# Kernel optimization log

Hardware: AMD Instinct MI355X
Metric: run time of the kernel (lower is better)

## Reference

```python
import jax, jax.numpy as jnp
import numpy as np

EPS = 1e-5

def _layernorm(h, g, b):
    mu = jnp.mean(h, axis=-1, keepdims=True)
    var = jnp.mean(jnp.square(h - mu), axis=-1, keepdims=True)
    return (h - mu) * jax.lax.rsqrt(var + EPS) * g + b

def setup_inputs() -> dict:
    key = jax.random.key(0)
    ks = jax.random.split(key, 16)
    N, E, H = 100000, 500000, 128
    x = jax.random.normal(ks[0], (N, H), dtype=jnp.float32)
    edge_index = jax.random.randint(ks[1], (2, E), 0, N, dtype=jnp.int64)
    edge = jax.random.normal(ks[2], (E, H), dtype=jnp.float32)
    def lin(k, fan_in, fan_out):
        bound = 1.0 / np.sqrt(fan_in)
        k1, k2 = jax.random.split(k)
        W = jax.random.uniform(k1, (fan_in, fan_out), jnp.float32, -bound, bound)
        b = jax.random.uniform(k2, (fan_out,), jnp.float32, -bound, bound)
        return W, b
    W0, b0 = lin(ks[3], 3 * H, H)
    W1, b1 = lin(ks[4], H, H)
    W2, b2 = lin(ks[5], H, H)
    W3, b3 = lin(ks[6], H, 1)
    g0 = jnp.ones((H,), jnp.float32); be0 = jnp.zeros((H,), jnp.float32)
    g1 = jnp.ones((H,), jnp.float32); be1 = jnp.zeros((H,), jnp.float32)
    g2 = jnp.ones((H,), jnp.float32); be2 = jnp.zeros((H,), jnp.float32)
    return dict(x=x, edge_index=edge_index, edge=edge,
                W0=W0, b0=b0, g0=g0, be0=be0,
                W1=W1, b1=b1, g1=g1, be1=be1,
                W2=W2, b2=b2, g2=g2, be2=be2,
                W3=W3, b3=b3)

def reference(x, edge_index, edge, W0, b0, g0, be0, W1, b1, g1, be1, W2, b2, g2, be2, W3, b3):
    src, dst = edge_index[0], edge_index[1]
    # gather + concat: [E, 3*H]
    h = jnp.concatenate([x[src], x[dst], edge], axis=-1)
    h = jax.nn.relu(_layernorm(h @ W0 + b0, g0, be0))
    h = jax.nn.relu(_layernorm(h @ W1 + b1, g1, be1))
    h = jax.nn.relu(_layernorm(h @ W2 + b2, g2, be2))
    out = h @ W3 + b3  # [E, 1]
    return jnp.squeeze(out, axis=-1)
```

## Files before the change

### kernel.cpp

```cpp
#include <hip/hip_runtime.h>

typedef _Float16 f16;
typedef _Float16 f16x8 __attribute__((ext_vector_type(8)));
typedef _Float16 f16x4 __attribute__((ext_vector_type(4)));
typedef float    f32x4 __attribute__((ext_vector_type(4)));

static constexpr int H  = 128;
static constexpr int MT = 128;
static constexpr int PC = 40;
static constexpr int PA = 136;

__global__ __launch_bounds__(256, 2)
void edge_mlp_fused(const float* __restrict__ x,
                    const int* __restrict__ eidx,
                    const float* __restrict__ edge,
                    const float* __restrict__ W0, const float* __restrict__ b0,
                    const float* __restrict__ g0, const float* __restrict__ be0,
                    const float* __restrict__ W1, const float* __restrict__ b1,
                    const float* __restrict__ g1, const float* __restrict__ be1,
                    const float* __restrict__ W2, const float* __restrict__ b2,
                    const float* __restrict__ g2, const float* __restrict__ be2,
                    const float* __restrict__ W3, const float* __restrict__ b3,
                    float* __restrict__ out, int E)
{
    __shared__ f16   achunk[MT * PC];
    __shared__ f16   wchunk[H * PC];
    __shared__ f16   act[MT * PA];
    __shared__ int   srcoff[MT];
    __shared__ int   dstoff[MT];
    __shared__ float outbuf[MT];

    const int tid  = threadIdx.x;
    const int lane = tid & 63;
    const int wid  = tid >> 6;
    const int c    = lane & 15;
    const int g    = lane >> 4;
    const int wrow = wid * 32;
    const long long e0 = (long long)blockIdx.x * MT;

    if (tid < MT) {
        long long e = e0 + tid; if (e >= E) e = (long long)E - 1;
        srcoff[tid] = eidx[e]     * (H * 4);
        dstoff[tid] = eidx[E + e] * (H * 4);
    }

    f32x4 acc[8][2];
    #pragma unroll
    for (int t = 0; t < 8; ++t) {
        acc[t][0] = f32x4{0.f, 0.f, 0.f, 0.f};
        acc[t][1] = f32x4{0.f, 0.f, 0.f, 0.f};
    }

    auto stageW = [&](const float* __restrict__ W, int k0) {
        #pragma unroll
        for (int i = 0; i < 4; ++i) {
            int f  = i * 256 + tid;
            int n  = f & 127;
            int kq = f >> 7;
            const float* p = W + (size_t)(k0 + kq * 4) * H + n;
            f16x4 v;
            v[0] = (f16)p[0];
            v[1] = (f16)p[H];
            v[2] = (f16)p[2 * H];
            v[3] = (f16)p[3 * H];
            *(f16x4*)&wchunk[n * PC + kq * 4] = v;
        }
    };

    auto mfma_tiles = [&](const f16* __restrict__ A, int astride, int koff) {
        f16x8 a0 = *(const f16x8*)&A[(wrow + c)      * astride + koff + g * 8];
        f16x8 a1 = *(const f16x8*)&A[(wrow + 16 + c) * astride + koff + g * 8];
        #pragma unroll
        for (int t = 0; t < 8; ++t) {
            f16x8 bf = *(const f16x8*)&wchunk[(t * 16 + c) * PC + g * 8];
            acc[t][0] = __builtin_amdgcn_mfma_f32_16x16x32_f16(a0, bf, acc[t][0], 0, 0, 0);
            acc[t][1] = __builtin_amdgcn_mfma_f32_16x16x32_f16(a1, bf, acc[t][1], 0, 0, 0);
        }
    };

    auto ln_relu_store = [&](const float* __restrict__ bias,
                             const float* __restrict__ gamma,
                             const float* __restrict__ beta) {
        float mu[2][4], rs[2][4];
        #pragma unroll
        for (int t = 0; t < 8; ++t) {
            float bt = bias[t * 16 + c];
            #pragma unroll
            for (int s = 0; s < 2; ++s)
                #pragma unroll
                for (int r = 0; r < 4; ++r) acc[t][s][r] += bt;
        }
        #pragma unroll
        for (int s = 0; s < 2; ++s)
            #pragma unroll
            for (int r = 0; r < 4; ++r) {
                float v = 0.f, q = 0.f;
                #pragma unroll
                for (int t = 0; t < 8; ++t) { float a = acc[t][s][r]; v += a; q += a * a; }
                #pragma unroll
                for (int m = 1; m < 16; m <<= 1) {
                    v += __shfl_xor(v, m, 64);
                    q += __shfl_xor(q, m, 64);
                }
                float mean = v * (1.0f / H);
                float var  = q * (1.0f / H) - mean * mean;
                mu[s][r] = mean;
                rs[s][r] = rsqrtf(var + 1e-5f);
            }
        __syncthreads();
        #pragma unroll
        for (int t = 0; t < 8; ++t) {
            float gm = gamma[t * 16 + c];
            float bb = beta[t * 16 + c];
            #pragma unroll
            for (int s = 0; s < 2; ++s)
                #pragma unroll
                for (int r = 0; r < 4; ++r) {
                    float v = (acc[t][s][r] - mu[s][r]) * rs[s][r] * gm + bb;
                    v = fmaxf(v, 0.f);
                    act[(wrow + s * 16 + g * 4 + r) * PA + t * 16 + c] = (f16)v;
                }
        }
        #pragma unroll
        for (int t = 0; t < 8; ++t) {
            acc[t][0] = f32x4{0.f, 0.f, 0.f, 0.f};
            acc[t][1] = f32x4{0.f, 0.f, 0.f, 0.f};
        }
    };

    for (int kc = 0; kc < 12; ++kc) {
        __syncthreads();
        {
            int r  = tid >> 1;
            int hf = tid & 1;
            int kk = (kc & 3) * 32 + hf * 16;
            const float* p;
            if (kc < 4)      p = (const float*)((const char*)x + srcoff[r]) + kk;
            else if (kc < 8) p = (const float*)((const char*)x + dstoff[r]) + kk;
            else {
                long long e = e0 + r; if (e >= E) e = (long long)E - 1;
                p = edge + e * H + kk;
            }
            float4 v0 = ((const float4*)p)[0];
            float4 v1 = ((const float4*)p)[1];
            float4 v2 = ((const float4*)p)[2];
            float4 v3 = ((const float4*)p)[3];
            f16x8 lo, hi;
            lo[0] = (f16)v0.x; lo[1] = (f16)v0.y; lo[2] = (f16)v0.z; lo[3] = (f16)v0.w;
            lo[4] = (f16)v1.x; lo[5] = (f16)v1.y; lo[6] = (f16)v1.z; lo[7] = (f16)v1.w;
            hi[0] = (f16)v2.x; hi[1] = (f16)v2.y; hi[2] = (f16)v2.z; hi[3] = (f16)v2.w;
            hi[4] = (f16)v3.x; hi[5] = (f16)v3.y; hi[6] = (f16)v3.z; hi[7] = (f16)v3.w;
            *(f16x8*)&achunk[r * PC + hf * 16]     = lo;
            *(f16x8*)&achunk[r * PC + hf * 16 + 8] = hi;
        }
        stageW(W0, kc * 32);
        __syncthreads();
        mfma_tiles(achunk, PC, 0);
    }
    ln_relu_store(b0, g0, be0);

    for (int kc = 0; kc < 4; ++kc) {
        __syncthreads();
        stageW(W1, kc * 32);
        __syncthreads();
        mfma_tiles(act, PA, kc * 32);
    }
    ln_relu_store(b1, g1, be1);

    for (int kc = 0; kc < 4; ++kc) {
        __syncthreads();
        stageW(W2, kc * 32);
        __syncthreads();
        mfma_tiles(act, PA, kc * 32);
    }

    {
        float mu[2][4], rs[2][4];
        #pragma unroll
        for (int t = 0; t < 8; ++t) {
            float bt = b2[t * 16 + c];
            #pragma unroll
            for (int s = 0; s < 2; ++s)
                #pragma unroll
                for (int r = 0; r < 4; ++r) acc[t][s][r] += bt;
        }
        #pragma unroll
        for (int s = 0; s < 2; ++s)
            #pragma unroll
            for (int r = 0; r < 4; ++r) {
                float v = 0.f, q = 0.f;
                #pragma unroll
                for (int t = 0; t < 8; ++t) { float a = acc[t][s][r]; v += a; q += a * a; }
                #pragma unroll
                for (int m = 1; m < 16; m <<= 1) {
                    v += __shfl_xor(v, m, 64);
                    q += __shfl_xor(q, m, 64);
                }
                float mean = v * (1.0f / H);
                float var  = q * (1.0f / H) - mean * mean;
                mu[s][r] = mean;
                rs[s][r] = rsqrtf(var + 1e-5f);
            }
        float po[2][4] = {{0.f,0.f,0.f,0.f},{0.f,0.f,0.f,0.f}};
        #pragma unroll
        for (int t = 0; t < 8; ++t) {
            float gm  = g2[t * 16 + c];
            float bb  = be2[t * 16 + c];
            float w3v = W3[t * 16 + c];
            #pragma unroll
            for (int s = 0; s < 2; ++s)
                #pragma unroll
                for (int r = 0; r < 4; ++r) {
                    float v = (acc[t][s][r] - mu[s][r]) * rs[s][r] * gm + bb;
                    v = fmaxf(v, 0.f);
                    po[s][r] += v * w3v;
                }
        }
        #pragma unroll
        for (int s = 0; s < 2; ++s)
            #pragma unroll
            for (int r = 0; r < 4; ++r) {
                #pragma unroll
                for (int m = 1; m < 16; m <<= 1) po[s][r] += __shfl_xor(po[s][r], m, 64);
            }
        if (c == 0) {
            #pragma unroll
            for (int s = 0; s < 2; ++s)
                #pragma unroll
                for (int r = 0; r < 4; ++r)
                    outbuf[wrow + s * 16 + g * 4 + r] = po[s][r];
        }
    }
    __syncthreads();
    if (tid < MT) {
        long long e = e0 + tid;
        if (e < E) out[e] = outbuf[tid] + b3[0];
    }
}

extern "C" void kernel_launch(void* const* d_in, const int* in_sizes, int n_in,
                              void* d_out, int out_size, void* d_ws, size_t ws_size,
                              hipStream_t stream)
{
    const float* x    = (const float*)d_in[0];
    const int*   eidx = (const int*)d_in[1];
    const float* edge = (const float*)d_in[2];
    const float* W0   = (const float*)d_in[3];
    const float* b0   = (const float*)d_in[4];
    const float* g0   = (const float*)d_in[5];
    const float* be0  = (const float*)d_in[6];
    const float* W1   = (const float*)d_in[7];
    const float* b1   = (const float*)d_in[8];
    const float* g1   = (const float*)d_in[9];
    const float* be1  = (const float*)d_in[10];
    const float* W2   = (const float*)d_in[11];
    const float* b2   = (const float*)d_in[12];
    const float* g2   = (const float*)d_in[13];
    const float* be2  = (const float*)d_in[14];
    const float* W3   = (const float*)d_in[15];
    const float* b3   = (const float*)d_in[16];
    float*       out  = (float*)d_out;

    const int E = in_sizes[1] / 2;
    const int grid = (E + MT - 1) / MT;

    hipLaunchKernelGGL(edge_mlp_fused, dim3(grid), dim3(256), 0, stream,
                       x, eidx, edge,
                       W0, b0, g0, be0,
                       W1, b1, g1, be1,
                       W2, b2, g2, be2,
                       W3, b3, out, E);
}
```

Baseline: 576.5 us.

## Pre-transpose weights to fp16 and load operands directly into MFMA registers

A small prep kernel converts W0-W2 to transposed fp16 in workspace once per launch. The main kernel then drops the per-block LDS staging of weights and gathered inputs: each lane loads its A fragments from global x/edge rows and its B fragments from the fp16 weights straight into registers. This removes most __syncthreads and shrinks shared memory, so occupancy can rise to 4 blocks per CU. The cost is an extra launch and uncached, less coalesced global B-fragment reads that depend on L1/L2 hits.

Measured after the change: 850.2 us. 47.5% more time.

```diff
diff --git a/kernel.cpp b/kernel.cpp
--- a/kernel.cpp
+++ b/kernel.cpp
@@ -1,34 +1,49 @@
 #include <hip/hip_runtime.h>
 
 typedef _Float16 f16;
+typedef _Float16 f16x4 __attribute__((ext_vector_type(4)));
 typedef _Float16 f16x8 __attribute__((ext_vector_type(8)));
-typedef _Float16 f16x4 __attribute__((ext_vector_type(4)));
 typedef float    f32x4 __attribute__((ext_vector_type(4)));
 
 static constexpr int H  = 128;
 static constexpr int MT = 128;
-static constexpr int PC = 40;
 static constexpr int PA = 136;
-
-__global__ __launch_bounds__(256, 2)
-void edge_mlp_fused(const float* __restrict__ x,
-                    const int* __restrict__ eidx,
-                    const float* __restrict__ edge,
-                    const float* __restrict__ W0, const float* __restrict__ b0,
-                    const float* __restrict__ g0, const float* __restrict__ be0,
-                    const float* __restrict__ W1, const float* __restrict__ b1,
-                    const float* __restrict__ g1, const float* __restrict__ be1,
-                    const float* __restrict__ W2, const float* __restrict__ b2,
-                    const float* __restrict__ g2, const float* __restrict__ be2,
-                    const float* __restrict__ W3, const float* __restrict__ b3,
-                    float* __restrict__ out, int E)
+static constexpr int W0T_OFF = 0;
+static constexpr int W1T_OFF = 128 * 384;
+static constexpr int W2T_OFF = 128 * 384 + 128 * 128;
+
+__global__ __launch_bounds__(256)
+void prep_weights(const float* __restrict__ W0,
+                  const float* __restrict__ W1,
+                  const float* __restrict__ W2,
+                  f16* __restrict__ o)
 {
-    __shared__ f16   achunk[MT * PC];
-    __shared__ f16   wchunk[H * PC];
-    __shared__ f16   act[MT * PA];
-    __shared__ int   srcoff[MT];
-    __shared__ int   dstoff[MT];
-    __shared__ float outbuf[MT];
+    int tid = blockIdx.x * 256 + threadIdx.x;
+    const float* W; f16* dst; int K, idx;
+    if (tid < 12288)      { W = W0; dst = o + W0T_OFF; K = 384; idx = tid; }
+    else if (tid < 16384) { W = W1; dst = o + W1T_OFF; K = 128; idx = tid - 12288; }
+    else if (tid < 20480) { W = W2; dst = o + W2T_OFF; K = 128; idx = tid - 16384; }
+    else return;
+    int n  = idx & 127;
+    int k4 = idx >> 7;
+    f16x4 v;
+    #pragma unroll
+    for (int j = 0; j < 4; ++j) v[j] = (f16)W[(k4 * 4 + j) * H + n];
+    *(f16x4*)&dst[n * K + k4 * 4] = v;
+}
+
+__global__ __launch_bounds__(256, 4)
+void edge_mlp(const float* __restrict__ x,
+              const int* __restrict__ eidx,
+              const float* __restrict__ edge,
+              const f16* __restrict__ wsW,
+              const float* __restrict__ b0, const float* __restrict__ g0, const float* __restrict__ be0,
+              const float* __restrict__ b1, const float* __restrict__ g1, const float* __restrict__ be1,
+              const float* __restrict__ b2, const float* __restrict__ g2, const float* __restrict__ be2,
+              const float* __restrict__ W3, const float* __restrict__ b3,
+              float* __restrict__ out, int E)
+{
+    __shared__ f16 act[MT * PA];
 
     const int tid  = threadIdx.x;
     const int lane = tid & 63;
@@ -38,11 +53,14 @@
     const int wrow = wid * 32;
     const long long e0 = (long long)blockIdx.x * MT;
 
-    if (tid < MT) {
-        long long e = e0 + tid; if (e >= E) e = (long long)E - 1;
-        srcoff[tid] = eidx[e]     * (H * 4);
-        dstoff[tid] = eidx[E + e] * (H * 4);
-    }
+    long long ea = e0 + wrow + c;      if (ea >= E) ea = (long long)E - 1;
+    long long eb = e0 + wrow + 16 + c; if (eb >= E) eb = (long long)E - 1;
+    const float* sp0 = x + (size_t)eidx[ea] * H;
+    const float* sp1 = x + (size_t)eidx[eb] * H;
+    const float* dp0 = x + (size_t)eidx[E + ea] * H;
+    const float* dp1 = x + (size_t)eidx[E + eb] * H;
+    const float* ep0 = edge + (size_t)ea * H;
+    const float* ep1 = edge + (size_t)eb * H;
 
     f32x4 acc[8][2];
     #pragma unroll
@@ -51,28 +69,19 @@
         acc[t][1] = f32x4{0.f, 0.f, 0.f, 0.f};
     }
 
-    auto stageW = [&](const float* __restrict__ W, int k0) {
-        #pragma unroll
-        for (int i = 0; i < 4; ++i) {
-            int f  = i * 256 + tid;
-            int n  = f & 127;
-            int kq = f >> 7;
-            const float* p = W + (size_t)(k0 + kq * 4) * H + n;
-            f16x4 v;
-            v[0] = (f16)p[0];
-            v[1] = (f16)p[H];
-            v[2] = (f16)p[2 * H];
-            v[3] = (f16)p[3 * H];
-            *(f16x4*)&wchunk[n * PC + kq * 4] = v;
-        }
+    auto load_a = [&](const float* p, int off) -> f16x8 {
+        float4 u = *(const float4*)(p + off);
+        float4 v = *(const float4*)(p + off + 4);
+        f16x8 a;
+        a[0] = (f16)u.x; a[1] = (f16)u.y; a[2] = (f16)u.z; a[3] = (f16)u.w;
+        a[4] = (f16)v.x; a[5] = (f16)v.y; a[6] = (f16)v.z; a[7] = (f16)v.w;
+        return a;
     };
 
-    auto mfma_tiles = [&](const f16* __restrict__ A, int astride, int koff) {
-        f16x8 a0 = *(const f16x8*)&A[(wrow + c)      * astride + koff + g * 8];
-        f16x8 a1 = *(const f16x8*)&A[(wrow + 16 + c) * astride + koff + g * 8];
-        #pragma unroll
-        for (int t = 0; t < 8; ++t) {
-            f16x8 bf = *(const f16x8*)&wchunk[(t * 16 + c) * PC + g * 8];
+    auto mfma_step = [&](f16x8 a0, f16x8 a1, const f16* wt, int Kh, int koff) {
+        #pragma unroll
+        for (int t = 0; t < 8; ++t) {
+            f16x8 bf = *(const f16x8*)&wt[(size_t)(t * 16 + c) * Kh + koff + g * 8];
             acc[t][0] = __builtin_amdgcn_mfma_f32_16x16x32_f16(a0, bf, acc[t][0], 0, 0, 0);
             acc[t][1] = __builtin_amdgcn_mfma_f32_16x16x32_f16(a1, bf, acc[t][1], 0, 0, 0);
         }
@@ -107,7 +116,6 @@
                 mu[s][r] = mean;
                 rs[s][r] = rsqrtf(var + 1e-5f);
             }
-        __syncthreads();
         #pragma unroll
         for (int t = 0; t < 8; ++t) {
             float gm = gamma[t * 16 + c];
@@ -128,50 +136,39 @@
         }
     };
 
-    for (int kc = 0; kc < 12; ++kc) {
-        __syncthreads();
-        {
-            int r  = tid >> 1;
-            int hf = tid & 1;
-            int kk = (kc & 3) * 32 + hf * 16;
-            const float* p;
-            if (kc < 4)      p = (const float*)((const char*)x + srcoff[r]) + kk;
-            else if (kc < 8) p = (const float*)((const char*)x + dstoff[r]) + kk;
-            else {
-                long long e = e0 + r; if (e >= E) e = (long long)E - 1;
-                p = edge + e * H + kk;
-            }
-            float4 v0 = ((const float4*)p)[0];
-            float4 v1 = ((const float4*)p)[1];
-            float4 v2 = ((const float4*)p)[2];
-            float4 v3 = ((const float4*)p)[3];
-            f16x8 lo, hi;
-            lo[0] = (f16)v0.x; lo[1] = (f16)v0.y; lo[2] = (f16)v0.z; lo[3] = (f16)v0.w;
-            lo[4] = (f16)v1.x; lo[5] = (f16)v1.y; lo[6] = (f16)v1.z; lo[7] = (f16)v1.w;
-            hi[0] = (f16)v2.x; hi[1] = (f16)v2.y; hi[2] = (f16)v2.z; hi[3] = (f16)v2.w;
-            hi[4] = (f16)v3.x; hi[5] = (f16)v3.y; hi[6] = (f16)v3.z; hi[7] = (f16)v3.w;
-            *(f16x8*)&achunk[r * PC + hf * 16]     = lo;
-            *(f16x8*)&achunk[r * PC + hf * 16 + 8] = hi;
-        }
-        stageW(W0, kc * 32);
-        __syncthreads();
-        mfma_tiles(achunk, PC, 0);
+    const f16* w0t = wsW + W0T_OFF;
+    #pragma unroll
+    for (int kc = 0; kc < 4; ++kc) {
+        int off = kc * 32 + g * 8;
+        mfma_step(load_a(sp0, off), load_a(sp1, off), w0t, 384, kc * 32);
+    }
+    #pragma unroll
+    for (int kc = 0; kc < 4; ++kc) {
+        int off = kc * 32 + g * 8;
+        mfma_step(load_a(dp0, off), load_a(dp1, off), w0t, 384, 128 + kc * 32);
+    }
+    #pragma unroll
+    for (int kc = 0; kc < 4; ++kc) {
+        int off = kc * 32 + g * 8;
+        mfma_step(load_a(ep0, off), load_a(ep1, off), w0t, 384, 256 + kc * 32);
     }
     ln_relu_store(b0, g0, be0);
 
-    for (int kc = 0; kc < 4; ++kc) {
-        __syncthreads();
-        stageW(W1, kc * 32);
-        __syncthreads();
-        mfma_tiles(act, PA, kc * 32);
+    const f16* w1t = wsW + W1T_OFF;
+    #pragma unroll
+    for (int kc = 0; kc < 4; ++kc) {
+        f16x8 a0 = *(const f16x8*)&act[(wrow + c) * PA + kc * 32 + g * 8];
+        f16x8 a1 = *(const f16x8*)&act[(wrow + 16 + c) * PA + kc * 32 + g * 8];
+        mfma_step(a0, a1, w1t, 128, kc * 32);
     }
     ln_relu_store(b1, g1, be1);
 
-    for (int kc = 0; kc < 4; ++kc) {
-        __syncthreads();
-        stageW(W2, kc * 32);
-        __syncthreads();
-        mfma_tiles(act, PA, kc * 32);
+    const f16* w2t = wsW + W2T_OFF;
+    #pragma unroll
+    for (int kc = 0; kc < 4; ++kc) {
+        f16x8 a0 = *(const f16x8*)&act[(wrow + c) * PA + kc * 32 + g * 8];
+        f16x8 a1 = *(const f16x8*)&act[(wrow + 16 + c) * PA + kc * 32 + g * 8];
+        mfma_step(a0, a1, w2t, 128, kc * 32);
     }
 
     {
@@ -216,6 +213,7 @@
                     po[s][r] += v * w3v;
                 }
         }
+        float b3v = b3[0];
         #pragma unroll
         for (int s = 0; s < 2; ++s)
             #pragma unroll
@@ -227,14 +225,11 @@
             #pragma unroll
             for (int s = 0; s < 2; ++s)
                 #pragma unroll
-                for (int r = 0; r < 4; ++r)
-                    outbuf[wrow + s * 16 + g * 4 + r] = po[s][r];
-        }
-    }
-    __syncthreads();
-    if (tid < MT) {
-        long long e = e0 + tid;
-        if (e < E) out[e] = outbuf[tid] + b3[0];
+                for (int r = 0; r < 4; ++r) {
+                    long long e = e0 + wrow + s * 16 + g * 4 + r;
+                    if (e < E) out[e] = po[s][r] + b3v;
+                }
+        }
     }
 }
 
@@ -260,14 +255,16 @@
     const float* W3   = (const float*)d_in[15];
     const float* b3   = (const float*)d_in[16];
     float*       out  = (float*)d_out;
+    f16*         wsW  = (f16*)d_ws;
 
     const int E = in_sizes[1] / 2;
     const int grid = (E + MT - 1) / MT;
 
-    hipLaunchKernelGGL(edge_mlp_fused, dim3(grid), dim3(256), 0, stream,
-                       x, eidx, edge,
-                       W0, b0, g0, be0,
-                       W1, b1, g1, be1,
-                       W2, b2, g2, be2,
+    hipLaunchKernelGGL(prep_weights, dim3(80), dim3(256), 0, stream, W0, W1, W2, wsW);
+    hipLaunchKernelGGL(edge_mlp, dim3(grid), dim3(256), 0, stream,
+                       x, eidx, edge, wsW,
+                       b0, g0, be0,
+                       b1, g1, be1,
+                       b2, g2, be2,
                        W3, b3, out, E);
 }
```
